# Optimization experiments

Hardware: AMD Instinct MI355X
Metric: run time of the kernel (lower is better)

The kernel has to match this reference:

```python
import jax, jax.numpy as jnp
import numpy as np

N_NODES = 100000
N_EDGES = 1000000
IN_FEAT = 64
OUT_FEAT = 64


def setup_inputs() -> dict:
    key = jax.random.key(0)
    ks = jax.random.split(key, 12)
    d, o = IN_FEAT, OUT_FEAT
    s = 1.0 / np.sqrt(d)
    s2 = 1.0 / np.sqrt(2 * d)
    return {
        "x": jax.random.normal(ks[0], (N_NODES, d), dtype=jnp.float32),
        "edge_index": jax.random.randint(ks[1], (2, N_EDGES), 0, N_NODES, dtype=jnp.int64),
        "batch": jnp.zeros((N_NODES,), dtype=jnp.int64),
        # message MLP: Linear(d,d) -> ReLU -> Linear(d,d)
        "msg_w1": jax.random.uniform(ks[2], (d, d), jnp.float32, -s, s),
        "msg_b1": jax.random.uniform(ks[3], (d,), jnp.float32, -s, s),
        "msg_w2": jax.random.uniform(ks[4], (d, d), jnp.float32, -s, s),
        "msg_b2": jax.random.uniform(ks[5], (d,), jnp.float32, -s, s),
        # output MLP: Linear(2d,d) -> ReLU -> Linear(d,out)
        "out_w1": jax.random.uniform(ks[6], (2 * d, d), jnp.float32, -s2, s2),
        "out_b1": jax.random.uniform(ks[7], (d,), jnp.float32, -s2, s2),
        "out_w2": jax.random.uniform(ks[8], (d, o), jnp.float32, -s, s),
        "out_b2": jax.random.uniform(ks[9], (o,), jnp.float32, -s, s),
    }


def reference(x, edge_index, batch, msg_w1, msg_b1, msg_w2, msg_b2,
              out_w1, out_b1, out_w2, out_b2):
    row, col = edge_index[0], edge_index[1]
    # gather source-node features per edge, apply message MLP
    h = x[row]                                   # [E, d]
    msg = jax.nn.relu(h @ msg_w1 + msg_b1) @ msg_w2 + msg_b2  # [E, d]
    # force processor: node features pass through as fx; scatter-sum messages
    fx = x                                        # [N, d]
    agg = jax.ops.segment_sum(msg, col, num_segments=N_NODES)  # [N, d]
    out_final = jnp.concatenate([fx, agg], axis=1)  # [N, 2d]
    out = jax.nn.relu(out_final @ out_w1 + out_b1) @ out_w2 + out_b2  # [N, out]
    return out
```

## Files before the change

kernel.cpp:

```cpp
#include <hip/hip_runtime.h>
#include <hip/hip_bf16.h>

#define D 64
#define BSHIFT 7
#define BW (1 << BSHIFT)
#define MAXB 1024
#define CAP 8192
#define STRIDE 4096

typedef __attribute__((ext_vector_type(8))) short bf16x8;
typedef __attribute__((ext_vector_type(4))) float f32x4;

__device__ __forceinline__ short f2bf(float f) {
    __hip_bfloat16 h = __float2bfloat16(f);
    return *reinterpret_cast<short*>(&h);
}

__global__ __launch_bounds__(256) void msg_kernel(
    const float* __restrict__ x,
    const float* __restrict__ w1, const float* __restrict__ b1,
    const float* __restrict__ w2, const float* __restrict__ b2,
    __hip_bfloat16* __restrict__ m, int n_nodes)
{
    __shared__ __align__(16) __hip_bfloat16 sH[4][16 * 72];

    const int lane = threadIdx.x & 63;
    const int wslot = threadIdx.x >> 6;
    const int mr   = lane & 15;
    const int quad = lane >> 4;

    bf16x8 w1f[2][4], w2f[2][4];
    float  b1v[4], b2v[4];
#pragma unroll
    for (int ks = 0; ks < 2; ++ks)
#pragma unroll
        for (int nb = 0; nb < 4; ++nb) {
            bf16x8 f1, f2;
#pragma unroll
            for (int j = 0; j < 8; ++j) {
                int k = ks * 32 + quad * 8 + j;
                f1[j] = f2bf(w1[k * D + nb * 16 + mr]);
                f2[j] = f2bf(w2[k * D + nb * 16 + mr]);
            }
            w1f[ks][nb] = f1;
            w2f[ks][nb] = f2;
        }
#pragma unroll
    for (int nb = 0; nb < 4; ++nb) {
        b1v[nb] = b1[nb * 16 + mr];
        b2v[nb] = b2[nb * 16 + mr];
    }

    __hip_bfloat16* Hw = sH[wslot];
    const int wid    = (blockIdx.x * blockDim.x + threadIdx.x) >> 6;
    const int nwaves = (gridDim.x * blockDim.x) >> 6;
    const int ntiles = (n_nodes + 15) >> 4;

    for (int t = wid; t < ntiles; t += nwaves) {
        const int v0 = t * 16;
        int vr = v0 + mr;
        if (vr >= n_nodes) vr = n_nodes - 1;

        bf16x8 a[2];
#pragma unroll
        for (int ks = 0; ks < 2; ++ks) {
            const float* p = x + (size_t)vr * D + ks * 32 + quad * 8;
            float4 lo = *(const float4*)p;
            float4 hi = *(const float4*)(p + 4);
            bf16x8 f;
            f[0] = f2bf(lo.x); f[1] = f2bf(lo.y); f[2] = f2bf(lo.z); f[3] = f2bf(lo.w);
            f[4] = f2bf(hi.x); f[5] = f2bf(hi.y); f[6] = f2bf(hi.z); f[7] = f2bf(hi.w);
            a[ks] = f;
        }

#pragma unroll
        for (int nb = 0; nb < 4; ++nb) {
            f32x4 acc = {0.f, 0.f, 0.f, 0.f};
            acc = __builtin_amdgcn_mfma_f32_16x16x32_bf16(a[0], w1f[0][nb], acc, 0, 0, 0);
            acc = __builtin_amdgcn_mfma_f32_16x16x32_bf16(a[1], w1f[1][nb], acc, 0, 0, 0);
#pragma unroll
            for (int r = 0; r < 4; ++r) {
                float hv = fmaxf(acc[r] + b1v[nb], 0.f);
                Hw[(quad * 4 + r) * 72 + nb * 16 + mr] = __float2bfloat16(hv);
            }
        }

        bf16x8 h[2];
#pragma unroll
        for (int ks = 0; ks < 2; ++ks)
            h[ks] = *(const bf16x8*)&Hw[mr * 72 + ks * 32 + quad * 8];

#pragma unroll
        for (int nb = 0; nb < 4; ++nb) {
            f32x4 acc = {0.f, 0.f, 0.f, 0.f};
            acc = __builtin_amdgcn_mfma_f32_16x16x32_bf16(h[0], w2f[0][nb], acc, 0, 0, 0);
            acc = __builtin_amdgcn_mfma_f32_16x16x32_bf16(h[1], w2f[1][nb], acc, 0, 0, 0);
#pragma unroll
            for (int r = 0; r < 4; ++r)
                Hw[(quad * 4 + r) * 72 + nb * 16 + mr] =
                    __float2bfloat16(acc[r] + b2v[nb]);
        }

#pragma unroll
        for (int s = 0; s < 2; ++s) {
            const int rrow = s * 8 + (lane >> 3);
            const int cblk = (lane & 7) * 8;
            bf16x8 val = *(const bf16x8*)&Hw[rrow * 72 + cblk];
            const int vrow = v0 + rrow;
            if (vrow < n_nodes)
                *(bf16x8*)&m[(size_t)vrow * D + cblk] = val;
        }
    }
}

__global__ __launch_bounds__(256) void bin_kernel(
    const int* __restrict__ row, const int* __restrict__ col,
    int* __restrict__ gcur, unsigned int* __restrict__ tmp,
    int n_edges, int nbuckets, int chunk)
{
    __shared__ int hist[MAXB], base[MAXB], lcur[MAXB];
    const int t = threadIdx.x;
    const int e0 = blockIdx.x * chunk;
    const int e1 = min(e0 + chunk, n_edges);

    for (int i = t; i < nbuckets; i += 256) hist[i] = 0;
    __syncthreads();
    for (int e = e0 + t; e < e1; e += 256)
        atomicAdd(&hist[col[e] >> BSHIFT], 1);
    __syncthreads();
    for (int i = t; i < nbuckets; i += 256) {
        base[i] = hist[i] ? atomicAdd(&gcur[i], hist[i]) : 0;
        lcur[i] = 0;
    }
    __syncthreads();
    for (int e = e0 + t; e < e1; e += 256) {
        int c = col[e];
        int b = c >> BSHIFT;
        int loc = base[b] + atomicAdd(&lcur[b], 1);
        if (loc < STRIDE) {
            unsigned int val = ((unsigned int)(c & (BW - 1)) << 17)
                             | (unsigned int)row[e];
            tmp[(size_t)b * STRIDE + loc] = val;
        }
    }
}

__global__ __launch_bounds__(1024) void bucket_gather_kernel(
    const int* __restrict__ gcur, const unsigned int* __restrict__ tmp,
    const __hip_bfloat16* __restrict__ m, __hip_bfloat16* __restrict__ agg,
    int n_nodes, int nbuckets)
{
    __shared__ unsigned int sorted[CAP];
    __shared__ int cnt[BW], off[BW], cur[BW];

    const int b    = blockIdx.x;
    const int t    = threadIdx.x;
    const int lane = t & 63;
    const int wv   = t >> 6;
    const int vbase = b << BSHIFT;
    const unsigned int* gtmp = tmp + (size_t)b * STRIDE;

    const int total = min(gcur[b], STRIDE);

    float acc[8];
#pragma unroll
    for (int i = 0; i < 8; ++i) acc[i] = 0.f;

    for (int r0 = 0; r0 < total; r0 += CAP) {
        const int r1 = min(r0 + CAP, total);

        if (t < BW) cnt[t] = 0;
        __syncthreads();

        for (int i = r0 + t; i < r1; i += 1024)
            atomicAdd(&cnt[gtmp[i] >> 17], 1);
        __syncthreads();

        if (t < BW) off[t] = cnt[t];
        __syncthreads();
        for (int d = 1; d < BW; d <<= 1) {
            int u = 0;
            if (t < BW && t >= d) u = off[t - d];
            __syncthreads();
            if (t < BW) off[t] += u;
            __syncthreads();
        }
        if (t < BW) {
            int e = off[t] - cnt[t];
            off[t] = e;
            cur[t] = e;
        }
        __syncthreads();

        for (int i = r0 + t; i < r1; i += 1024) {
            unsigned int u = gtmp[i];
            int pos = atomicAdd(&cur[u >> 17], 1);
            sorted[pos] = u;
        }
        __syncthreads();

#pragma unroll
        for (int i = 0; i < 8; ++i) {
            const int n  = wv + (i << 4);
            const int o0 = off[n];
            const int c  = cnt[n];
            float s = 0.f;
            for (int cs = 0; cs < c; cs += 64) {
                const int k = min(64, c - cs);
                unsigned int pv = 0;
                if (lane < k) pv = sorted[o0 + cs + lane];

                int j = 0;
                for (; j + 8 <= k; j += 8) {
                    unsigned int u[8];
                    float v[8];
#pragma unroll
                    for (int q = 0; q < 8; ++q)
                        u[q] = __builtin_amdgcn_readlane(pv, j + q);
#pragma unroll
                    for (int q = 0; q < 8; ++q)
                        v[q] = (float)m[(size_t)(u[q] & 0x1FFFFu) * D + lane];
#pragma unroll
                    for (int q = 0; q < 8; ++q)
                        s += v[q];
                }
                for (; j < k; ++j) {
                    unsigned int u = __builtin_amdgcn_readlane(pv, j);
                    s += (float)m[(size_t)(u & 0x1FFFFu) * D + lane];
                }
            }
            acc[i] += s;
        }
        __syncthreads();
    }

#pragma unroll
    for (int i = 0; i < 8; ++i) {
        const int v = vbase + wv + (i << 4);
        if (v < n_nodes)
            agg[(size_t)v * D + lane] = __float2bfloat16(acc[i]);
    }
}

__global__ __launch_bounds__(256) void scatter_kernel(
    const int* __restrict__ row, const int* __restrict__ col,
    const __hip_bfloat16* __restrict__ m, float* __restrict__ aggf, int n_edges)
{
    const int lane = threadIdx.x & 63;
    const int wid  = (blockIdx.x * blockDim.x + threadIdx.x) >> 6;
    const int base = wid * 64;
    if (base >= n_edges) return;
    const int cnt = min(64, n_edges - base);

    int my_r = 0, my_c = 0;
    if (lane < cnt) { my_r = row[base + lane]; my_c = col[base + lane]; }

    for (int j = 0; j < cnt; ++j) {
        int r = __builtin_amdgcn_readlane(my_r, j);
        int c = __builtin_amdgcn_readlane(my_c, j);
        float v = (float)m[(size_t)r * D + lane];
        atomicAdd(&aggf[(size_t)c * D + lane], v);
    }
}

__global__ __launch_bounds__(256) void cvt_kernel(
    const float* __restrict__ aggf, __hip_bfloat16* __restrict__ agg, int n)
{
    int i = blockIdx.x * blockDim.x + threadIdx.x;
    if (i < n) agg[i] = __float2bfloat16(aggf[i]);
}

__global__ __launch_bounds__(256) void out_kernel(
    const float* __restrict__ x, const __hip_bfloat16* __restrict__ agg,
    const float* __restrict__ w1, const float* __restrict__ b1,
    const float* __restrict__ w2, const float* __restrict__ b2,
    float* __restrict__ out, int n_nodes)
{
    __shared__ __align__(16) __hip_bfloat16 sH[4][16 * 72];

    const int lane = threadIdx.x & 63;
    const int wslot = threadIdx.x >> 6;
    const int mr   = lane & 15;
    const int quad = lane >> 4;

    bf16x8 w1f[4][4], w2f[2][4];
    float  b1v[4], b2v[4];
#pragma unroll
    for (int ks = 0; ks < 4; ++ks)
#pragma unroll
        for (int nb = 0; nb < 4; ++nb) {
            bf16x8 f;
#pragma unroll
            for (int j = 0; j < 8; ++j) {
                int k = ks * 32 + quad * 8 + j;
                f[j] = f2bf(w1[k * D + nb * 16 + mr]);
            }
            w1f[ks][nb] = f;
        }
#pragma unroll
    for (int ks = 0; ks < 2; ++ks)
#pragma unroll
        for (int nb = 0; nb < 4; ++nb) {
            bf16x8 f;
#pragma unroll
            for (int j = 0; j < 8; ++j) {
                int k = ks * 32 + quad * 8 + j;
                f[j] = f2bf(w2[k * D + nb * 16 + mr]);
            }
            w2f[ks][nb] = f;
        }
#pragma unroll
    for (int nb = 0; nb < 4; ++nb) {
        b1v[nb] = b1[nb * 16 + mr];
        b2v[nb] = b2[nb * 16 + mr];
    }

    __hip_bfloat16* Hw = sH[wslot];
    const int wid    = (blockIdx.x * blockDim.x + threadIdx.x) >> 6;
    const int nwaves = (gridDim.x * blockDim.x) >> 6;
    const int ntiles = (n_nodes + 15) >> 4;

    for (int t = wid; t < ntiles; t += nwaves) {
        const int v0 = t * 16;
        int vr = v0 + mr;
        if (vr >= n_nodes) vr = n_nodes - 1;

        bf16x8 a[4];
#pragma unroll
        for (int ks = 0; ks < 2; ++ks) {
            const float* p = x + (size_t)vr * D + ks * 32 + quad * 8;
            float4 lo = *(const float4*)p;
            float4 hi = *(const float4*)(p + 4);
            bf16x8 f;
            f[0] = f2bf(lo.x); f[1] = f2bf(lo.y); f[2] = f2bf(lo.z); f[3] = f2bf(lo.w);
            f[4] = f2bf(hi.x); f[5] = f2bf(hi.y); f[6] = f2bf(hi.z); f[7] = f2bf(hi.w);
            a[ks] = f;
        }
#pragma unroll
        for (int ks = 2; ks < 4; ++ks)
            a[ks] = *(const bf16x8*)&agg[(size_t)vr * D + (ks - 2) * 32 + quad * 8];

#pragma unroll
        for (int nb = 0; nb < 4; ++nb) {
            f32x4 acc = {0.f, 0.f, 0.f, 0.f};
#pragma unroll
            for (int ks = 0; ks < 4; ++ks)
                acc = __builtin_amdgcn_mfma_f32_16x16x32_bf16(a[ks], w1f[ks][nb], acc, 0, 0, 0);
#pragma unroll
            for (int r = 0; r < 4; ++r) {
                float hv = fmaxf(acc[r] + b1v[nb], 0.f);
                Hw[(quad * 4 + r) * 72 + nb * 16 + mr] = __float2bfloat16(hv);
            }
        }

        bf16x8 h[2];
#pragma unroll
        for (int ks = 0; ks < 2; ++ks)
            h[ks] = *(const bf16x8*)&Hw[mr * 72 + ks * 32 + quad * 8];

#pragma unroll
        for (int nb = 0; nb < 4; ++nb) {
            f32x4 acc = {0.f, 0.f, 0.f, 0.f};
            acc = __builtin_amdgcn_mfma_f32_16x16x32_bf16(h[0], w2f[0][nb], acc, 0, 0, 0);
            acc = __builtin_amdgcn_mfma_f32_16x16x32_bf16(h[1], w2f[1][nb], acc, 0, 0, 0);
#pragma unroll
            for (int r = 0; r < 4; ++r) {
                int vrow = v0 + quad * 4 + r;
                if (vrow < n_nodes)
                    out[(size_t)vrow * D + nb * 16 + mr] = acc[r] + b2v[nb];
            }
        }
    }
}

extern "C" void kernel_launch(void* const* d_in, const int* in_sizes, int n_in,
                              void* d_out, int out_size, void* d_ws, size_t ws_size,
                              hipStream_t stream) {
    const float* x   = (const float*)d_in[0];
    const int*   ei  = (const int*)d_in[1];
    const float* mw1 = (const float*)d_in[3];
    const float* mb1 = (const float*)d_in[4];
    const float* mw2 = (const float*)d_in[5];
    const float* mb2 = (const float*)d_in[6];
    const float* ow1 = (const float*)d_in[7];
    const float* ob1 = (const float*)d_in[8];
    const float* ow2 = (const float*)d_in[9];
    const float* ob2 = (const float*)d_in[10];

    const int n_nodes = in_sizes[0] / D;
    const int n_edges = in_sizes[1] / 2;
    const int* row = ei;
    const int* col = ei + n_edges;

    const int nbuckets = (n_nodes + BW - 1) >> BSHIFT;

    __hip_bfloat16* m   = (__hip_bfloat16*)d_ws;
    __hip_bfloat16* agg = m + (size_t)n_nodes * D;
    unsigned int* tmp   = (unsigned int*)(agg + (size_t)n_nodes * D);
    const size_t region = (size_t)nbuckets * STRIDE * 4 > (size_t)n_nodes * D * 4
                        ? (size_t)nbuckets * STRIDE * 4 : (size_t)n_nodes * D * 4;
    int* gcur = (int*)((char*)tmp + region);
    float* aggf = (float*)tmp;
    const size_t need = (size_t)n_nodes * D * 4 + region + (size_t)nbuckets * 4;

    const int ntiles = (n_nodes + 15) / 16;
    int nblk = (ntiles + 3) / 4;
    if (nblk > 512) nblk = 512;

    msg_kernel<<<nblk, 256, 0, stream>>>(x, mw1, mb1, mw2, mb2, m, n_nodes);

    const bool shape_ok = (n_nodes < (1 << 17)) && (nbuckets <= MAXB)
                       && (n_edges <= nbuckets * (STRIDE / 2));

    if (ws_size >= need && shape_ok) {
        hipMemsetAsync(gcur, 0, (size_t)nbuckets * sizeof(int), stream);
        const int nbbin = 128;
        const int chunk = (n_edges + nbbin - 1) / nbbin;
        bin_kernel<<<nbbin, 256, 0, stream>>>(row, col, gcur, tmp,
                                              n_edges, nbuckets, chunk);
        bucket_gather_kernel<<<nbuckets, 1024, 0, stream>>>(gcur, tmp, m, agg,
                                                            n_nodes, nbuckets);
    } else {
        hipMemsetAsync(aggf, 0, (size_t)n_nodes * D * sizeof(float), stream);
        const int nwaves_s = (n_edges + 63) / 64;
        scatter_kernel<<<(nwaves_s + 3) / 4, 256, 0, stream>>>(row, col, m, aggf, n_edges);
        cvt_kernel<<<((n_nodes * D) + 255) / 256, 256, 0, stream>>>(aggf, agg, n_nodes * D);
    }

    out_kernel<<<nblk, 256, 0, stream>>>(x, agg, ow1, ob1, ow2, ob2,
                                         (float*)d_out, n_nodes);
}
```

Before: 194.3 us.

## Fuse output MLP into bucket gather kernel to skip agg round-trip

The bucket gather kernel now applies the output MLP (concat with x, two bf16 MFMA layers) right after aggregating each 128-node bucket. The aggregate stays in shared memory instead of being written to global memory and read back by a separate out_kernel launch. Each of the roughly 782 blocks reloads and converts both output weight matrices into fragment layout in LDS, which adds per-block overhead. Only 8 of the 16 waves do the MLP work.

```diff
diff --git a/kernel.cpp b/kernel.cpp
--- a/kernel.cpp
+++ b/kernel.cpp
@@ -145,13 +145,21 @@
     }
 }
 
-__global__ __launch_bounds__(1024) void bucket_gather_kernel(
+__global__ __launch_bounds__(1024) void bucket_gather_out_kernel(
     const int* __restrict__ gcur, const unsigned int* __restrict__ tmp,
-    const __hip_bfloat16* __restrict__ m, __hip_bfloat16* __restrict__ agg,
-    int n_nodes, int nbuckets)
+    const __hip_bfloat16* __restrict__ m, const float* __restrict__ x,
+    const float* __restrict__ w1, const float* __restrict__ b1,
+    const float* __restrict__ w2, const float* __restrict__ b2,
+    float* __restrict__ out, int n_nodes, int nbuckets)
 {
-    __shared__ unsigned int sorted[CAP];
+    __shared__ __align__(16) char shreg[(128 * 72 + 8 * 16 * 72) * 2];
+    __shared__ __align__(16) __hip_bfloat16 sW1f[16 * 512];
+    __shared__ __align__(16) __hip_bfloat16 sW2f[8 * 512];
     __shared__ int cnt[BW], off[BW], cur[BW];
+
+    unsigned int* sorted = (unsigned int*)shreg;
+    __hip_bfloat16* sH  = (__hip_bfloat16*)shreg;
+    __hip_bfloat16* sH2 = (__hip_bfloat16*)shreg + 128 * 72;
 
     const int b    = blockIdx.x;
     const int t    = threadIdx.x;
@@ -159,6 +167,19 @@
     const int wv   = t >> 6;
     const int vbase = b << BSHIFT;
     const unsigned int* gtmp = tmp + (size_t)b * STRIDE;
+
+    for (int i = t; i < 16 * 512; i += 1024) {
+        int frag = i >> 9, ln = (i >> 3) & 63, j = i & 7;
+        int k = (frag >> 2) * 32 + ((ln >> 4) << 3) + j;
+        int c = (frag & 3) * 16 + (ln & 15);
+        sW1f[i] = __float2bfloat16(w1[k * D + c]);
+    }
+    for (int i = t; i < 8 * 512; i += 1024) {
+        int frag = i >> 9, ln = (i >> 3) & 63, j = i & 7;
+        int k = (frag >> 2) * 32 + ((ln >> 4) << 3) + j;
+        int c = (frag & 3) * 16 + (ln & 15);
+        sW2f[i] = __float2bfloat16(w2[k * D + c]);
+    }
 
     const int total = min(gcur[b], STRIDE);
 
@@ -235,10 +256,75 @@
     }
 
 #pragma unroll
-    for (int i = 0; i < 8; ++i) {
-        const int v = vbase + wv + (i << 4);
-        if (v < n_nodes)
-            agg[(size_t)v * D + lane] = __float2bfloat16(acc[i]);
+    for (int i = 0; i < 8; ++i)
+        sH[(wv + (i << 4)) * 72 + lane] = __float2bfloat16(acc[i]);
+    __syncthreads();
+
+    if (wv < 8) {
+        const int tt = wv;
+        const int mr = lane & 15;
+        const int quad = lane >> 4;
+        int vr = vbase + tt * 16 + mr;
+        if (vr >= n_nodes) vr = n_nodes - 1;
+
+        bf16x8 a[4];
+#pragma unroll
+        for (int ks = 0; ks < 2; ++ks) {
+            const float* p = x + (size_t)vr * D + ks * 32 + quad * 8;
+            float4 lo = *(const float4*)p;
+            float4 hi = *(const float4*)(p + 4);
+            bf16x8 f;
+            f[0] = f2bf(lo.x); f[1] = f2bf(lo.y); f[2] = f2bf(lo.z); f[3] = f2bf(lo.w);
+            f[4] = f2bf(hi.x); f[5] = f2bf(hi.y); f[6] = f2bf(hi.z); f[7] = f2bf(hi.w);
+            a[ks] = f;
+        }
+#pragma unroll
+        for (int ks = 2; ks < 4; ++ks)
+            a[ks] = *(const bf16x8*)&sH[(tt * 16 + mr) * 72 + (ks - 2) * 32 + quad * 8];
+
+        float b1v[4], b2v[4];
+#pragma unroll
+        for (int nb = 0; nb < 4; ++nb) {
+            b1v[nb] = b1[nb * 16 + mr];
+            b2v[nb] = b2[nb * 16 + mr];
+        }
+
+        __hip_bfloat16* H2 = sH2 + tt * 16 * 72;
+#pragma unroll
+        for (int nb = 0; nb < 4; ++nb) {
+            f32x4 c4 = {0.f, 0.f, 0.f, 0.f};
+#pragma unroll
+            for (int ks = 0; ks < 4; ++ks) {
+                bf16x8 wf = *(const bf16x8*)&sW1f[(ks * 4 + nb) * 512 + lane * 8];
+                c4 = __builtin_amdgcn_mfma_f32_16x16x32_bf16(a[ks], wf, c4, 0, 0, 0);
+            }
+#pragma unroll
+            for (int r = 0; r < 4; ++r) {
+                float hv = fmaxf(c4[r] + b1v[nb], 0.f);
+                H2[(quad * 4 + r) * 72 + nb * 16 + mr] = __float2bfloat16(hv);
+            }
+        }
+
+        bf16x8 h[2];
+#pragma unroll
+        for (int ks = 0; ks < 2; ++ks)
+            h[ks] = *(const bf16x8*)&H2[mr * 72 + ks * 32 + quad * 8];
+
+#pragma unroll
+        for (int nb = 0; nb < 4; ++nb) {
+            f32x4 c4 = {0.f, 0.f, 0.f, 0.f};
+#pragma unroll
+            for (int ks = 0; ks < 2; ++ks) {
+                bf16x8 wf = *(const bf16x8*)&sW2f[(ks * 4 + nb) * 512 + lane * 8];
+                c4 = __builtin_amdgcn_mfma_f32_16x16x32_bf16(h[ks], wf, c4, 0, 0, 0);
+            }
+#pragma unroll
+            for (int r = 0; r < 4; ++r) {
+                int vrow = vbase + tt * 16 + quad * 4 + r;
+                if (vrow < n_nodes)
+                    out[(size_t)vrow * D + nb * 16 + mr] = c4[r] + b2v[nb];
+            }
+        }
     }
 }
 
@@ -418,15 +504,15 @@
         const int chunk = (n_edges + nbbin - 1) / nbbin;
         bin_kernel<<<nbbin, 256, 0, stream>>>(row, col, gcur, tmp,
                                               n_edges, nbuckets, chunk);
-        bucket_gather_kernel<<<nbuckets, 1024, 0, stream>>>(gcur, tmp, m, agg,
-                                                            n_nodes, nbuckets);
+        bucket_gather_out_kernel<<<nbuckets, 1024, 0, stream>>>(
+            gcur, tmp, m, x, ow1, ob1, ow2, ob2,
+            (float*)d_out, n_nodes, nbuckets);
     } else {
         hipMemsetAsync(aggf, 0, (size_t)n_nodes * D * sizeof(float), stream);
         const int nwaves_s = (n_edges + 63) / 64;
         scatter_kernel<<<(nwaves_s + 3) / 4, 256, 0, stream>>>(row, col, m, aggf, n_edges);
         cvt_kernel<<<((n_nodes * D) + 255) / 256, 256, 0, stream>>>(aggf, agg, n_nodes * D);
-    }
-
-    out_kernel<<<nblk, 256, 0, stream>>>(x, agg, ow1, ob1, ow2, ob2,
-                                         (float*)d_out, n_nodes);
-}
+        out_kernel<<<nblk, 256, 0, stream>>>(x, agg, ow1, ob1, ow2, ob2,
+                                             (float*)d_out, n_nodes);
+    }
+}
```

Result: slower. 202.9 us (+4.4%).
